# Kernel tuning notes

Hardware: AMD Instinct MI355X
Metric: run time of the kernel (lower is better)

## Reference

```python
import jax, jax.numpy as jnp
import numpy as np

N, D, M1, K = 16384, 128, 64, 8  # batch, nodes (dims[0]), dims[1], k


def setup_inputs() -> dict:
    key = jax.random.key(0)
    ks = jax.random.split(key, 8)
    x = jax.random.normal(ks[0], (N, D), dtype=jnp.float32)
    # Stacked per-node fc1 weights: d independent Linear(d, m1) layers.
    s = 0.1
    w1_pos = jax.random.normal(ks[1], (D, M1, D), dtype=jnp.float32) * s
    b1_pos = jax.random.normal(ks[2], (D, M1), dtype=jnp.float32) * s
    w1_neg = jax.random.normal(ks[3], (D, M1, D), dtype=jnp.float32) * s
    b1_neg = jax.random.normal(ks[4], (D, M1), dtype=jnp.float32) * s
    # LocallyConnected(K, M1, 1): weight [K, M1, 1], bias [K, 1]
    w2 = jax.random.normal(ks[5], (K, M1, 1), dtype=jnp.float32) * s
    b2 = jax.random.normal(ks[6], (K, 1), dtype=jnp.float32) * s
    # fc3: d independent Linear(K, 1, bias=False) -> stacked [D, K]
    w3 = jax.random.normal(ks[7], (D, K), dtype=jnp.float32) * s
    return {"x": x, "w1_pos": w1_pos, "b1_pos": b1_pos,
            "w1_neg": w1_neg, "b1_neg": b1_neg,
            "w2": w2, "b2": b2, "w3": w3}


def reference(x, w1_pos, b1_pos, w1_neg, b1_neg, w2, b2, w3):
    d = x.shape[1]
    # Zeroing x[:, j] for node j == zeroing column j of node-j fc1 weight.
    mask = 1.0 - jnp.eye(d, dtype=x.dtype)            # [d, d]
    W = (w1_pos - w1_neg) * mask[:, None, :]          # [d, m1, d]
    b = b1_pos - b1_neg                                # [d, m1]
    h = jnp.einsum('nd,jmd->njm', x, W) + b            # [n, d, m1]
    # expand over K then sigmoid (sigmoid is identical for each k copy)
    h = jax.nn.sigmoid(h)
    # LocallyConnected: per-k matmul [m1 -> 1], bias [K, 1]
    z = jnp.einsum('njm,kmo->njko', h, w2) + b2        # [n, d, K, 1]
    z = z[..., 0]                                       # [n, d, K]
    # fc3: per-node Linear(K, 1, bias=False)
    out = jnp.einsum('njk,jk->nj', z, w3)              # [n, d]
    return out
```

## Files before the change

kernel.cpp:

```cpp
#include <hip/hip_runtime.h>

#define N_  16384
#define D_  128
#define M1_ 64
#define K_  8
#define LOG2E 1.44269504088896f

typedef short short8 __attribute__((ext_vector_type(8)));
typedef float f32x4  __attribute__((ext_vector_type(4)));

__device__ __forceinline__ unsigned cvt_pk_bf16(float lo, float hi) {
    unsigned r;
    asm("v_cvt_pk_bf16_f32 %0, %1, %2" : "=v"(r) : "v"(lo), "v"(hi));
    return r;
}

__global__ void prep_all(const float* __restrict__ x,
                         const float* __restrict__ w1p, const float* __restrict__ b1p,
                         const float* __restrict__ w1n, const float* __restrict__ b1n,
                         const float* __restrict__ w2,  const float* __restrict__ b2,
                         const float* __restrict__ w3,
                         ushort* __restrict__ xbf, ushort* __restrict__ wbf,
                         float* __restrict__ bp, float* __restrict__ vv,
                         float* __restrict__ cv) {
    int bx = blockIdx.x;
    if (bx < 1024) {
        int g    = bx * 256 + threadIdx.x;
        int lane = g & 63;
        int ks   = (g >> 6) & 3;
        int n16  = g >> 8;
        int row   = n16 * 16 + (lane & 15);
        int dbase = ks * 32 + (lane >> 4) * 8;
        const float* xp = x + (size_t)row * D_ + dbase;
        float4 a = *(const float4*)xp;
        float4 b = *(const float4*)(xp + 4);
        union { unsigned u[4]; short8 s; } r;
        r.u[0] = cvt_pk_bf16(a.x, a.y);
        r.u[1] = cvt_pk_bf16(a.z, a.w);
        r.u[2] = cvt_pk_bf16(b.x, b.y);
        r.u[3] = cvt_pk_bf16(b.z, b.w);
        *(short8*)&xbf[(size_t)g * 8] = r.s;
    } else if (bx < 1536) {
        int g    = (bx - 1024) * 256 + threadIdx.x;
        int lane = g & 63;
        int t    = (g >> 6) & 15;
        int j    = g >> 10;
        int ks = t >> 2, mt = t & 3;
        int m     = mt * 16 + (lane & 15);
        int dbase = ks * 32 + (lane >> 4) * 8;
        const float* pp = w1p + ((size_t)(j * M1_ + m)) * D_ + dbase;
        const float* np = w1n + ((size_t)(j * M1_ + m)) * D_ + dbase;
        float4 p0 = *(const float4*)pp;
        float4 p1 = *(const float4*)(pp + 4);
        float4 n0 = *(const float4*)np;
        float4 n1 = *(const float4*)(np + 4);
        float f[8];
        f[0] = (p0.x - n0.x) * LOG2E; f[1] = (p0.y - n0.y) * LOG2E;
        f[2] = (p0.z - n0.z) * LOG2E; f[3] = (p0.w - n0.w) * LOG2E;
        f[4] = (p1.x - n1.x) * LOG2E; f[5] = (p1.y - n1.y) * LOG2E;
        f[6] = (p1.z - n1.z) * LOG2E; f[7] = (p1.w - n1.w) * LOG2E;
        #pragma unroll
        for (int e = 0; e < 8; e++)
            if (dbase + e == j) f[e] = 0.f;
        union { unsigned u[4]; short8 s; } r;
        r.u[0] = cvt_pk_bf16(f[0], f[1]);
        r.u[1] = cvt_pk_bf16(f[2], f[3]);
        r.u[2] = cvt_pk_bf16(f[4], f[5]);
        r.u[3] = cvt_pk_bf16(f[6], f[7]);
        *(short8*)&wbf[(size_t)g * 8] = r.s;
    } else {
        int idx = (bx - 1536) * 256 + threadIdx.x;
        int j = idx >> 6, m = idx & 63;
        float v = 0.f;
        for (int k = 0; k < K_; k++) v += w3[j * K_ + k] * w2[k * M1_ + m];
        vv[idx] = v;
        bp[idx] = (b1p[idx] - b1n[idx]) * LOG2E;
        if (m == 0) {
            float c = 0.f;
            for (int k = 0; k < K_; k++) c += w3[j * K_ + k] * b2[k];
            cv[j] = c;
        }
    }
}

__global__ __launch_bounds__(256) void main_mfma(
    const ushort* __restrict__ xbf, const ushort* __restrict__ wbf,
    const float* __restrict__ bvec, const float* __restrict__ vvec,
    const float* __restrict__ cvec, float* __restrict__ out) {
    const int tid  = threadIdx.x;
    const int wave = tid >> 6, lane = tid & 63;
    const int quad = lane >> 4, col = lane & 15;
    const int j    = blockIdx.y;
    const int nblk = blockIdx.x;

    short8 wfrag[4][4];
    const ushort* wg = wbf + (size_t)j * 8192 + lane * 8;
    #pragma unroll
    for (int ks = 0; ks < 4; ks++)
        #pragma unroll
        for (int mt = 0; mt < 4; mt++)
            wfrag[mt][ks] = *(const short8*)&wg[(ks * 4 + mt) * 512];

    f32x4 bias4[4], vm4[4];
    #pragma unroll
    for (int mt = 0; mt < 4; mt++) {
        bias4[mt] = *(const f32x4*)&bvec[j * M1_ + mt * 16 + quad * 4];
        vm4[mt]   = *(const f32x4*)&vvec[j * M1_ + mt * 16 + quad * 4];
    }
    const float cj = cvec[j];

    const ushort* xg = xbf + ((size_t)(nblk * 32 + wave)) * 2048 + lane * 8;
    float* outp = out + (size_t)(nblk * 512 + wave * 16 + col) * D_ + j;

    short8 abuf[2][4];
    #pragma unroll
    for (int ks = 0; ks < 4; ks++)
        abuf[0][ks] = *(const short8*)&xg[ks * 512];

    float pr[8];

    #pragma unroll
    for (int st = 0; st < 8; st++) {
        const int cur = st & 1, nxt = cur ^ 1;
        if (st < 7) {
            const ushort* xn = xg + (size_t)(st + 1) * 8192;
            #pragma unroll
            for (int ks = 0; ks < 4; ks++)
                abuf[nxt][ks] = *(const short8*)&xn[ks * 512];
        }

        f32x4 acc[4];
        #pragma unroll
        for (int mt = 0; mt < 4; mt++) acc[mt] = bias4[mt];
        #pragma unroll
        for (int ks = 0; ks < 4; ks++)
            #pragma unroll
            for (int mt = 0; mt < 4; mt++)
                acc[mt] = __builtin_amdgcn_mfma_f32_16x16x32_bf16(
                              wfrag[mt][ks], abuf[cur][ks], acc[mt], 0, 0, 0);

        float partial = 0.f;
        #pragma unroll
        for (int mt = 0; mt < 4; mt++)
            #pragma unroll
            for (int r = 0; r < 4; r++) {
                float e = __builtin_amdgcn_exp2f(-acc[mt][r]);
                float s = __builtin_amdgcn_rcpf(1.0f + e);
                partial = fmaf(s, vm4[mt][r], partial);
            }
        pr[st] = partial;
    }

    #pragma unroll
    for (int st = 0; st < 8; st++)
        pr[st] += __shfl_xor(pr[st], 16);
    #pragma unroll
    for (int st = 0; st < 8; st++)
        pr[st] += __shfl_xor(pr[st], 32);
    if (quad == 0) {
        #pragma unroll
        for (int st = 0; st < 8; st++)
            outp[(size_t)st * 64 * D_] = pr[st] + cj;
    }
}

__global__ void fallback_kernel(const float* __restrict__ x,
                                const float* __restrict__ w1p, const float* __restrict__ b1p,
                                const float* __restrict__ w1n, const float* __restrict__ b1n,
                                const float* __restrict__ w2,  const float* __restrict__ b2,
                                const float* __restrict__ w3,  float* __restrict__ out) {
    int n = blockIdx.x, j = blockIdx.y, m = threadIdx.x;
    const float* xr = x + (size_t)n * D_;
    const float* wp = w1p + ((size_t)j * M1_ + m) * D_;
    const float* wn = w1n + ((size_t)j * M1_ + m) * D_;
    float acc = 0.f;
    for (int d = 0; d < D_; d++) {
        if (d == j) continue;
        acc += xr[d] * (wp[d] - wn[d]);
    }
    acc += b1p[j * M1_ + m] - b1n[j * M1_ + m];
    float h = 1.f / (1.f + __expf(-acc));
    float vmv = 0.f;
    for (int k = 0; k < K_; k++) vmv += w3[j * K_ + k] * w2[k * M1_ + m];
    float p = h * vmv;
    for (int off = 1; off < 64; off <<= 1) p += __shfl_xor(p, off);
    if (m == 0) {
        float c = 0.f;
        for (int k = 0; k < K_; k++) c += w3[j * K_ + k] * b2[k];
        out[(size_t)n * D_ + j] = p + c;
    }
}

extern "C" void kernel_launch(void* const* d_in, const int* in_sizes, int n_in,
                              void* d_out, int out_size, void* d_ws, size_t ws_size,
                              hipStream_t stream) {
    const float* x   = (const float*)d_in[0];
    const float* w1p = (const float*)d_in[1];
    const float* b1p = (const float*)d_in[2];
    const float* w1n = (const float*)d_in[3];
    const float* b1n = (const float*)d_in[4];
    const float* w2  = (const float*)d_in[5];
    const float* b2  = (const float*)d_in[6];
    const float* w3  = (const float*)d_in[7];
    float* out = (float*)d_out;

    const size_t off_x = 0;
    const size_t off_w = off_x + (size_t)N_ * D_ * 2;
    const size_t off_b = off_w + (size_t)D_ * M1_ * D_ * 2;
    const size_t off_v = off_b + (size_t)D_ * M1_ * 4;
    const size_t off_c = off_v + (size_t)D_ * M1_ * 4;
    const size_t need  = off_c + (size_t)D_ * 4;

    if (ws_size < need) {
        fallback_kernel<<<dim3(N_, D_), 64, 0, stream>>>(x, w1p, b1p, w1n, b1n, w2, b2, w3, out);
        return;
    }

    ushort* xbf = (ushort*)((char*)d_ws + off_x);
    ushort* wbf = (ushort*)((char*)d_ws + off_w);
    float*  bp  = (float*)((char*)d_ws + off_b);
    float*  vv  = (float*)((char*)d_ws + off_v);
    float*  cv  = (float*)((char*)d_ws + off_c);

    prep_all<<<1568, 256, 0, stream>>>(x, w1p, b1p, w1n, b1n, w2, b2, w3,
                                       xbf, wbf, bp, vv, cv);
    main_mfma<<<dim3(32, 128), 256, 0, stream>>>(xbf, wbf, bp, vv, cv, out);
}
```

Measured before the change: 124.3 us.

## Software-pipeline sigmoid epilogue behind next step's MFMAs and cap occupancy bound

```diff
diff --git a/kernel.cpp b/kernel.cpp
--- a/kernel.cpp
+++ b/kernel.cpp
@@ -83,7 +83,7 @@
     }
 }
 
-__global__ __launch_bounds__(256) void main_mfma(
+__global__ __launch_bounds__(256, 4) void main_mfma(
     const ushort* __restrict__ xbf, const ushort* __restrict__ wbf,
     const float* __restrict__ bvec, const float* __restrict__ vvec,
     const float* __restrict__ cvec, float* __restrict__ out) {
@@ -117,7 +117,27 @@
     for (int ks = 0; ks < 4; ks++)
         abuf[0][ks] = *(const short8*)&xg[ks * 512];
 
+    f32x4 acc[2][4];
     float pr[8];
+
+    #define EPILOGUE(A)                                                        \
+        ({ float pa_ = 0.f, pb_ = 0.f;                                         \
+           _Pragma("unroll")                                                   \
+           for (int r_ = 0; r_ < 4; r_++) {                                    \
+               float e0_ = __builtin_amdgcn_exp2f(-(A)[0][r_]);                \
+               float e1_ = __builtin_amdgcn_exp2f(-(A)[1][r_]);                \
+               float e2_ = __builtin_amdgcn_exp2f(-(A)[2][r_]);                \
+               float e3_ = __builtin_amdgcn_exp2f(-(A)[3][r_]);                \
+               float s0_ = __builtin_amdgcn_rcpf(1.0f + e0_);                  \
+               float s1_ = __builtin_amdgcn_rcpf(1.0f + e1_);                  \
+               float s2_ = __builtin_amdgcn_rcpf(1.0f + e2_);                  \
+               float s3_ = __builtin_amdgcn_rcpf(1.0f + e3_);                  \
+               pa_ = fmaf(s0_, vm4[0][r_], pa_);                               \
+               pb_ = fmaf(s1_, vm4[1][r_], pb_);                               \
+               pa_ = fmaf(s2_, vm4[2][r_], pa_);                               \
+               pb_ = fmaf(s3_, vm4[3][r_], pb_);                               \
+           }                                                                   \
+           pa_ + pb_; })
 
     #pragma unroll
     for (int st = 0; st < 8; st++) {
@@ -129,27 +149,20 @@
                 abuf[nxt][ks] = *(const short8*)&xn[ks * 512];
         }
 
-        f32x4 acc[4];
-        #pragma unroll
-        for (int mt = 0; mt < 4; mt++) acc[mt] = bias4[mt];
+        #pragma unroll
+        for (int mt = 0; mt < 4; mt++) acc[cur][mt] = bias4[mt];
         #pragma unroll
         for (int ks = 0; ks < 4; ks++)
             #pragma unroll
             for (int mt = 0; mt < 4; mt++)
-                acc[mt] = __builtin_amdgcn_mfma_f32_16x16x32_bf16(
-                              wfrag[mt][ks], abuf[cur][ks], acc[mt], 0, 0, 0);
-
-        float partial = 0.f;
-        #pragma unroll
-        for (int mt = 0; mt < 4; mt++)
-            #pragma unroll
-            for (int r = 0; r < 4; r++) {
-                float e = __builtin_amdgcn_exp2f(-acc[mt][r]);
-                float s = __builtin_amdgcn_rcpf(1.0f + e);
-                partial = fmaf(s, vm4[mt][r], partial);
-            }
-        pr[st] = partial;
-    }
+                acc[cur][mt] = __builtin_amdgcn_mfma_f32_16x16x32_bf16(
+                                   wfrag[mt][ks], abuf[cur][ks], acc[cur][mt], 0, 0, 0);
+
+        if (st >= 1)
+            pr[st - 1] = EPILOGUE(acc[nxt]);
+    }
+    pr[7] = EPILOGUE(acc[1]);
+    #undef EPILOGUE
 
     #pragma unroll
     for (int st = 0; st < 8; st++)
```

Result: slower. 341.5 us (+174.7%).

## Split M1 tiles across wave pairs and reduce partials through LDS

Applied to the files above, without the earlier changes.

```diff
diff --git a/kernel.cpp b/kernel.cpp
--- a/kernel.cpp
+++ b/kernel.cpp
@@ -83,34 +83,39 @@
     }
 }
 
-__global__ __launch_bounds__(256) void main_mfma(
+__global__ __launch_bounds__(256, 4) void main_mfma(
     const ushort* __restrict__ xbf, const ushort* __restrict__ wbf,
     const float* __restrict__ bvec, const float* __restrict__ vvec,
     const float* __restrict__ cvec, float* __restrict__ out) {
     const int tid  = threadIdx.x;
     const int wave = tid >> 6, lane = tid & 63;
     const int quad = lane >> 4, col = lane & 15;
+    const int mh   = wave & 1;
+    const int p    = wave >> 1;
     const int j    = blockIdx.y;
     const int nblk = blockIdx.x;
 
-    short8 wfrag[4][4];
+    __shared__ float lds_pr[4][8][64];
+
+    short8 wfrag[2][4];
     const ushort* wg = wbf + (size_t)j * 8192 + lane * 8;
     #pragma unroll
     for (int ks = 0; ks < 4; ks++)
         #pragma unroll
-        for (int mt = 0; mt < 4; mt++)
-            wfrag[mt][ks] = *(const short8*)&wg[(ks * 4 + mt) * 512];
-
-    f32x4 bias4[4], vm4[4];
-    #pragma unroll
-    for (int mt = 0; mt < 4; mt++) {
-        bias4[mt] = *(const f32x4*)&bvec[j * M1_ + mt * 16 + quad * 4];
-        vm4[mt]   = *(const f32x4*)&vvec[j * M1_ + mt * 16 + quad * 4];
+        for (int ml = 0; ml < 2; ml++)
+            wfrag[ml][ks] = *(const short8*)&wg[(ks * 4 + (mh * 2 + ml)) * 512];
+
+    f32x4 bias4[2], vm4[2];
+    #pragma unroll
+    for (int ml = 0; ml < 2; ml++) {
+        const int mb = j * M1_ + (mh * 2 + ml) * 16 + quad * 4;
+        bias4[ml] = *(const f32x4*)&bvec[mb];
+        vm4[ml]   = *(const f32x4*)&vvec[mb];
     }
     const float cj = cvec[j];
 
-    const ushort* xg = xbf + ((size_t)(nblk * 32 + wave)) * 2048 + lane * 8;
-    float* outp = out + (size_t)(nblk * 512 + wave * 16 + col) * D_ + j;
+    const ushort* xg = xbf + ((size_t)(nblk * 16 + p)) * 2048 + lane * 8;
+    float* outp = out + (size_t)(nblk * 256 + p * 16 + col) * D_ + j;
 
     short8 abuf[2][4];
     #pragma unroll
@@ -123,44 +128,56 @@
     for (int st = 0; st < 8; st++) {
         const int cur = st & 1, nxt = cur ^ 1;
         if (st < 7) {
-            const ushort* xn = xg + (size_t)(st + 1) * 8192;
+            const ushort* xn = xg + (size_t)(st + 1) * 4096;
             #pragma unroll
             for (int ks = 0; ks < 4; ks++)
                 abuf[nxt][ks] = *(const short8*)&xn[ks * 512];
         }
 
-        f32x4 acc[4];
-        #pragma unroll
-        for (int mt = 0; mt < 4; mt++) acc[mt] = bias4[mt];
-        #pragma unroll
-        for (int ks = 0; ks < 4; ks++)
+        f32x4 acc[2];
+        #pragma unroll
+        for (int ml = 0; ml < 2; ml++)
+            acc[ml] = __builtin_amdgcn_mfma_f32_16x16x32_bf16(
+                          wfrag[ml][0], abuf[cur][0], bias4[ml], 0, 0, 0);
+        #pragma unroll
+        for (int ks = 1; ks < 4; ks++)
             #pragma unroll
-            for (int mt = 0; mt < 4; mt++)
-                acc[mt] = __builtin_amdgcn_mfma_f32_16x16x32_bf16(
-                              wfrag[mt][ks], abuf[cur][ks], acc[mt], 0, 0, 0);
-
-        float partial = 0.f;
-        #pragma unroll
-        for (int mt = 0; mt < 4; mt++)
+            for (int ml = 0; ml < 2; ml++)
+                acc[ml] = __builtin_amdgcn_mfma_f32_16x16x32_bf16(
+                              wfrag[ml][ks], abuf[cur][ks], acc[ml], 0, 0, 0);
+
+        float pa = 0.f, pb = 0.f;
+        #pragma unroll
+        for (int r = 0; r < 4; r++) {
+            float e0 = __builtin_amdgcn_exp2f(-acc[0][r]);
+            float e1 = __builtin_amdgcn_exp2f(-acc[1][r]);
+            float s0 = __builtin_amdgcn_rcpf(1.0f + e0);
+            float s1 = __builtin_amdgcn_rcpf(1.0f + e1);
+            pa = fmaf(s0, vm4[0][r], pa);
+            pb = fmaf(s1, vm4[1][r], pb);
+        }
+        pr[st] = pa + pb;
+    }
+
+    #pragma unroll
+    for (int st = 0; st < 8; st++)
+        lds_pr[wave][st][lane] = pr[st];
+    __syncthreads();
+    if (mh == 0) {
+        #pragma unroll
+        for (int st = 0; st < 8; st++)
+            pr[st] += lds_pr[wave ^ 1][st][lane];
+        #pragma unroll
+        for (int st = 0; st < 8; st++)
+            pr[st] += __shfl_xor(pr[st], 16);
+        #pragma unroll
+        for (int st = 0; st < 8; st++)
+            pr[st] += __shfl_xor(pr[st], 32);
+        if (quad == 0) {
             #pragma unroll
-            for (int r = 0; r < 4; r++) {
-                float e = __builtin_amdgcn_exp2f(-acc[mt][r]);
-                float s = __builtin_amdgcn_rcpf(1.0f + e);
-                partial = fmaf(s, vm4[mt][r], partial);
-            }
-        pr[st] = partial;
-    }
-
-    #pragma unroll
-    for (int st = 0; st < 8; st++)
-        pr[st] += __shfl_xor(pr[st], 16);
-    #pragma unroll
-    for (int st = 0; st < 8; st++)
-        pr[st] += __shfl_xor(pr[st], 32);
-    if (quad == 0) {
-        #pragma unroll
-        for (int st = 0; st < 8; st++)
-            outp[(size_t)st * 64 * D_] = pr[st] + cj;
+            for (int st = 0; st < 8; st++)
+                outp[(size_t)st * 32 * D_] = pr[st] + cj;
+        }
     }
 }
 
@@ -224,5 +241,5 @@
 
     prep_all<<<1568, 256, 0, stream>>>(x, w1p, b1p, w1n, b1n, w2, b2, w3,
                                        xbf, wbf, bp, vv, cv);
-    main_mfma<<<dim3(32, 128), 256, 0, stream>>>(xbf, wbf, bp, vv, cv, out);
-}
+    main_mfma<<<dim3(64, 128), 256, 0, stream>>>(xbf, wbf, bp, vv, cv, out);
+}
```

Result: slower. 128.7 us (+3.5%).
